# Performance work log

Measured on AMD Instinct MI355X. Metric: run time of the kernel, lower is better.

## Reference

```python
import jax, jax.numpy as jnp
import numpy as np

E, H, W = 1024, 16, 256  # embed_dim, num_heads, window_size
D = E // H               # head_dim


def _rmsnorm(t, w):
    eps = jnp.finfo(t.dtype).eps
    return t * jax.lax.rsqrt(jnp.mean(t * t, axis=-1, keepdims=True) + eps) * w


def setup_inputs() -> dict:
    key = jax.random.key(0)
    ks = jax.random.split(key, 11)
    B, T = 2, 2048
    s = 1.0 / np.sqrt(E)
    return {
        "x": jax.random.normal(ks[0], (B, T, E), jnp.float32),
        "wq": jax.random.normal(ks[1], (E, E), jnp.float32) * s,
        "bq": jnp.zeros((E,), jnp.float32),
        "wk": jax.random.normal(ks[2], (E, E), jnp.float32) * s,
        "bk": jnp.zeros((E,), jnp.float32),
        "wv": jax.random.normal(ks[3], (E, E), jnp.float32) * s,
        "bv": jnp.zeros((E,), jnp.float32),
        "wo": jax.random.normal(ks[4], (E, E), jnp.float32) * s,
        "bo": jnp.zeros((E,), jnp.float32),
        "qn_w": jnp.ones((D,), jnp.float32),
        "kn_w": jnp.ones((D,), jnp.float32),
    }


def reference(x, wq, bq, wk, bk, wv, bv, wo, bo, qn_w, kn_w):
    B, T, _ = x.shape
    # projections; weights stored (in, out)
    q = (x @ wq + bq).reshape(B, T, H, D).transpose(0, 2, 1, 3)  # [B,H,T,D]
    k = (x @ wk + bk).reshape(B, T, H, D).transpose(0, 2, 1, 3)
    v = (x @ wv + bv).reshape(B, T, H, D).transpose(0, 2, 1, 3)
    q = _rmsnorm(q, qn_w)
    k = _rmsnorm(k, kn_w)

    scores = jnp.einsum("bhqd,bhkd->bhqk", q, k) / jnp.sqrt(jnp.float32(D))
    row = jnp.arange(T)[:, None]
    col = jnp.arange(T)[None, :]
    invalid = (col > row) | (row - col >= W)  # causal + sliding window
    neg_inf = jnp.float32(-jnp.inf)
    scores = jnp.where(invalid, neg_inf, scores)

    # genetic fitness reweighting
    masked_attn = jnp.where(invalid, 0.0, jax.nn.softmax(scores, axis=-1))
    gene_means = jnp.mean(jax.nn.sigmoid(masked_attn), axis=-1)  # [B,H,T]
    denom = gene_means + 0.5
    sum_inv = jnp.sum(1.0 / denom, axis=2, keepdims=True)        # [B,H,1]
    fitness = 1.0 / (denom * sum_inv)                            # [B,H,T]
    scores = scores + jnp.log(fitness)[..., None]

    attn = jax.nn.softmax(scores, axis=-1)
    out = jnp.einsum("bhqk,bhkd->bhqd", attn, v)
    out = out.transpose(0, 2, 1, 3).reshape(B, T, E)
    return out @ wo + bo
```

## Files before the change

### kernel.cpp

```cpp
#include <hip/hip_runtime.h>

typedef _Float16 f16;
typedef _Float16 f16x4 __attribute__((ext_vector_type(4)));
typedef _Float16 f16x8 __attribute__((ext_vector_type(8)));
typedef float f32x4 __attribute__((ext_vector_type(4)));

#define MFMA16(a, b, c) __builtin_amdgcn_mfma_f32_16x16x32_f16(a, b, c, 0, 0, 0)

constexpr int T = 2048;
constexpr int E = 1024;
constexpr int H = 16;
constexpr int D = 64;
constexpr int WIN = 256;
#define NEGF (-1e30f)
#define L2E 1.4426950408889634f

__device__ __forceinline__ void gload16(const f16* g, f16* l) {
  __builtin_amdgcn_global_load_lds(
      (__attribute__((address_space(1))) void*)(void*)g,
      (__attribute__((address_space(3))) void*)(void*)l, 16, 0, 0);
}

__global__ __launch_bounds__(256) void cast_x_kernel(const float* __restrict__ x,
                                                     f16* __restrict__ xb) {
  int idx = (blockIdx.x * 256 + threadIdx.x) * 4;
  float4 v = *(const float4*)(x + idx);
  f16x4 o = {(f16)v.x, (f16)v.y, (f16)v.z, (f16)v.w};
  *(f16x4*)(xb + idx) = o;
}

__global__ __launch_bounds__(256) void transpose_w_kernel(
    const float* __restrict__ w0, const float* __restrict__ w1,
    const float* __restrict__ w2, const float* __restrict__ w3,
    f16* __restrict__ o0, f16* __restrict__ o1, f16* __restrict__ o2,
    f16* __restrict__ o3) {
  int z = blockIdx.z;
  const float* w = z == 0 ? w0 : z == 1 ? w1 : z == 2 ? w2 : w3;
  f16* o = z == 0 ? o0 : z == 1 ? o1 : z == 2 ? o2 : o3;
  __shared__ float tile[64][65];
  int k0 = blockIdx.x * 64, n0 = blockIdx.y * 64;
  int r = threadIdx.x >> 2, cb = (threadIdx.x & 3) * 16;
  const float* src = w + (size_t)(k0 + r) * E + n0 + cb;
#pragma unroll
  for (int j = 0; j < 16; j += 4) {
    float4 v = *(const float4*)(src + j);
    tile[r][cb + j] = v.x;
    tile[r][cb + j + 1] = v.y;
    tile[r][cb + j + 2] = v.z;
    tile[r][cb + j + 3] = v.w;
  }
  __syncthreads();
  f16 tmp[16];
#pragma unroll
  for (int j = 0; j < 16; ++j) tmp[j] = (f16)tile[cb + j][r];
  f16* dst = o + (size_t)(n0 + r) * E + k0 + cb;
  *(f16x8*)dst = *(f16x8*)&tmp[0];
  *(f16x8*)(dst + 8) = *(f16x8*)&tmp[8];
}

template <int QKV>
__global__ __launch_bounds__(256) void gemm_bt_kernel(
    const f16* __restrict__ A, const f16* __restrict__ B0,
    const f16* __restrict__ B1, const f16* __restrict__ B2,
    const float* __restrict__ c0, const float* __restrict__ c1,
    const float* __restrict__ c2, const float* __restrict__ qnw,
    const float* __restrict__ knw, f16* __restrict__ oq, f16* __restrict__ ok,
    f16* __restrict__ Vt, float* __restrict__ of32, int M, int N, int K) {
  int z = blockIdx.z;
  const f16* Bt = z == 0 ? B0 : z == 1 ? B1 : B2;
  const float* bias = z == 0 ? c0 : z == 1 ? c1 : c2;

  __shared__ f16 lA[2][8192];
  __shared__ f16 lB[2][8192];

  int sw = ((blockIdx.x & 7) << 5) + (blockIdx.x >> 3);
  int m0 = (sw >> 3) << 7, n0 = (sw & 7) << 7;

  int tid = threadIdx.x;
  int wid = tid >> 6, lane = tid & 63;
  int wm = wid >> 1, wn = wid & 1;
  int lr = lane & 15, lg = lane >> 4;

  f32x4 zero = {0.f, 0.f, 0.f, 0.f};
  f32x4 acc[4][4];
  for (int a = 0; a < 4; ++a)
    for (int b = 0; b < 4; ++b) acc[a][b] = zero;

  int srow = lane >> 3;
  int scol = (lane & 7) << 3;

  auto stage = [&](int buf, int k0) {
#pragma unroll
    for (int p = 0; p < 4; ++p) {
      int cc = (wid << 2) + p;
      int row = (cc << 3) + srow;
      int gc = scol ^ ((row & 7) << 3);
      gload16(A + (size_t)(m0 + row) * K + k0 + gc, &lA[buf][cc << 9]);
      gload16(Bt + (size_t)(n0 + row) * K + k0 + gc, &lB[buf][cc << 9]);
    }
  };

  int nit = K >> 6;
  stage(0, 0);
  __syncthreads();
  int cur = 0;
  for (int t = 0; t < nit; ++t) {
    if (t + 1 < nit) stage(cur ^ 1, (t + 1) << 6);
#pragma unroll
    for (int kk = 0; kk < 2; ++kk) {
      int kc = kk * 32 + (lg << 3);
      f16x8 af[4], bf[4];
#pragma unroll
      for (int mt = 0; mt < 4; ++mt) {
        int row = wm * 64 + mt * 16 + lr;
        af[mt] = *(const f16x8*)&lA[cur][((row << 6) + kc) ^ ((row & 7) << 3)];
      }
#pragma unroll
      for (int nt = 0; nt < 4; ++nt) {
        int row = wn * 64 + nt * 16 + lr;
        bf[nt] = *(const f16x8*)&lB[cur][((row << 6) + kc) ^ ((row & 7) << 3)];
      }
#pragma unroll
      for (int mt = 0; mt < 4; ++mt)
#pragma unroll
        for (int nt = 0; nt < 4; ++nt)
          acc[mt][nt] = MFMA16(af[mt], bf[nt], acc[mt][nt]);
    }
    if (t + 1 < nit) {
      __syncthreads();
      cur ^= 1;
    }
  }

  if constexpr (QKV == 1) {
    if (z < 2) {
      const float* nw = z == 0 ? qnw : knw;
      f16* o = z == 0 ? oq : ok;
      const float eps = 1.1920929e-7f;
      const float osc = z == 0 ? 0.125f : 1.0f;
      float wv_[4];
#pragma unroll
      for (int nt = 0; nt < 4; ++nt) wv_[nt] = nw[nt * 16 + lr] * osc;
#pragma unroll
      for (int mt = 0; mt < 4; ++mt) {
        float vbuf[4][4];
        float ss[4] = {0.f, 0.f, 0.f, 0.f};
#pragma unroll
        for (int nt = 0; nt < 4; ++nt) {
          float bv = bias[n0 + wn * 64 + nt * 16 + lr];
#pragma unroll
          for (int i = 0; i < 4; ++i) {
            float v = acc[mt][nt][i] + bv;
            vbuf[nt][i] = v;
            ss[i] += v * v;
          }
        }
        float rr[4];
#pragma unroll
        for (int i = 0; i < 4; ++i) {
          ss[i] += __shfl_xor(ss[i], 1);
          ss[i] += __shfl_xor(ss[i], 2);
          ss[i] += __shfl_xor(ss[i], 4);
          ss[i] += __shfl_xor(ss[i], 8);
          rr[i] = rsqrtf(ss[i] * (1.0f / 64.0f) + eps);
        }
        int row = m0 + wm * 64 + mt * 16 + (lg << 2);
#pragma unroll
        for (int nt = 0; nt < 4; ++nt) {
          int col = n0 + wn * 64 + nt * 16 + lr;
#pragma unroll
          for (int i = 0; i < 4; ++i)
            o[(size_t)(row + i) * N + col] = (f16)(vbuf[nt][i] * rr[i] * wv_[nt]);
        }
      }
    } else {
#pragma unroll
      for (int mt = 0; mt < 4; ++mt) {
        int row = m0 + wm * 64 + mt * 16 + (lg << 2);
        int b = row >> 11;
        int t = row & (T - 1);
#pragma unroll
        for (int nt = 0; nt < 4; ++nt) {
          int col = n0 + wn * 64 + nt * 16 + lr;
          float bv = bias[col];
          int h = col >> 6, d = col & 63;
          f16x4 pk = {(f16)(acc[mt][nt][0] + bv), (f16)(acc[mt][nt][1] + bv),
                      (f16)(acc[mt][nt][2] + bv), (f16)(acc[mt][nt][3] + bv)};
          *(f16x4*)&Vt[(((size_t)(b * H + h) * D + d) << 11) + t] = pk;
        }
      }
    }
  } else {
#pragma unroll
    for (int mt = 0; mt < 4; ++mt) {
#pragma unroll
      for (int nt = 0; nt < 4; ++nt) {
        int row = m0 + wm * 64 + mt * 16 + (lg << 2);
        int col = n0 + wn * 64 + nt * 16 + lr;
        float bv = bias[col];
#pragma unroll
        for (int i = 0; i < 4; ++i)
          of32[(size_t)(row + i) * N + col] = acc[mt][nt][i] + bv;
      }
    }
  }
}

__global__ __launch_bounds__(256) void attn_kernel(const f16* __restrict__ qn,
                                                   const f16* __restrict__ kn,
                                                   const f16* __restrict__ Vt,
                                                   f16* __restrict__ aout) {
  int sw = ((blockIdx.x & 7) << 7) + (blockIdx.x >> 3);
  int q0 = (sw & 31) << 6;
  int bh = sw >> 5;
  int b = bh >> 4, h = bh & 15;
  int tid = threadIdx.x;
  int w = tid >> 6, lane = tid & 63;
  int lr = lane & 15, lg = lane >> 4;

  __shared__ f16 lK[2][4096];
  __shared__ f16 lV[2][4096];
  __shared__ f16 lP[4096];

  const f16* Qb = qn + (size_t)(b * T + q0 + w * 16 + lr) * E + h * 64 + (lg << 3);
  f16x8 qf0 = *(const f16x8*)Qb;
  f16x8 qf1 = *(const f16x8*)(Qb + 32);

  f32x4 zero = {0.f, 0.f, 0.f, 0.f};
  f32x4 acc[4] = {zero, zero, zero, zero};
  float m[4] = {NEGF, NEGF, NEGF, NEGF};
  float l[4] = {0.f, 0.f, 0.f, 0.f};

  int mi = q0 >> 6;
  int kts = mi - 4 < 0 ? 0 : mi - 4;

  const f16* Kbase = kn + (size_t)b * T * E + h * 64;
  const f16* Vbase = Vt + (size_t)bh * D * T;

  int srow = lane >> 3;
  int scol = (lane & 7) << 3;

  auto stageKV = [&](int buf, int kt) {
    int k0 = kt << 6;
#pragma unroll
    for (int p = 0; p < 2; ++p) {
      int cc = (w << 1) + p;
      int row = (cc << 3) + srow;
      int gc = scol ^ ((row & 7) << 3);
      gload16(Kbase + (size_t)(k0 + row) * E + gc, &lK[buf][cc << 9]);
      gload16(Vbase + (size_t)row * T + k0 + gc, &lV[buf][cc << 9]);
    }
  };

  stageKV(0, kts);
  __syncthreads();
  int cur = 0;

  for (int kt = kts; kt <= mi; ++kt) {
    if (kt < mi) stageKV(cur ^ 1, kt + 1);
    int k0 = kt << 6;

    f32x4 s[4];
#pragma unroll
    for (int ct = 0; ct < 4; ++ct) s[ct] = zero;
#pragma unroll
    for (int kk = 0; kk < 2; ++kk) {
      int kc = kk * 32 + (lg << 3);
#pragma unroll
      for (int ct = 0; ct < 4; ++ct) {
        int row = ct * 16 + lr;
        f16x8 bf = *(const f16x8*)&lK[cur][((row << 6) + kc) ^ ((row & 7) << 3)];
        s[ct] = MFMA16(kk == 0 ? qf0 : qf1, bf, s[ct]);
      }
    }

    float tm[4] = {NEGF, NEGF, NEGF, NEGF};
    int rowg0 = q0 + w * 16 + (lg << 2);
    bool needmask = (kt == mi) || (mi >= 4 && kt == kts);
    if (needmask) {
#pragma unroll
      for (int ct = 0; ct < 4; ++ct) {
        int col = k0 + ct * 16 + lr;
#pragma unroll
        for (int i = 0; i < 4; ++i) {
          int rowg = rowg0 + i;
          float v = s[ct][i];
          if (col > rowg || rowg - col >= WIN) v = NEGF;
          s[ct][i] = v;
          tm[i] = fmaxf(tm[i], v);
        }
      }
    } else {
#pragma unroll
      for (int ct = 0; ct < 4; ++ct)
#pragma unroll
        for (int i = 0; i < 4; ++i) tm[i] = fmaxf(tm[i], s[ct][i]);
    }
#pragma unroll
    for (int i = 0; i < 4; ++i) {
      tm[i] = fmaxf(tm[i], __shfl_xor(tm[i], 1));
      tm[i] = fmaxf(tm[i], __shfl_xor(tm[i], 2));
      tm[i] = fmaxf(tm[i], __shfl_xor(tm[i], 4));
      tm[i] = fmaxf(tm[i], __shfl_xor(tm[i], 8));
    }
    bool up = (tm[0] > m[0]) || (tm[1] > m[1]) || (tm[2] > m[2]) ||
              (tm[3] > m[3]);
    if (__any(up)) {
      float fac[4];
#pragma unroll
      for (int i = 0; i < 4; ++i) {
        float mn = fmaxf(m[i], tm[i]);
        fac[i] = exp2f((m[i] - mn) * L2E);
        m[i] = mn;
        l[i] *= fac[i];
      }
#pragma unroll
      for (int dt = 0; dt < 4; ++dt)
#pragma unroll
        for (int i = 0; i < 4; ++i) acc[dt][i] *= fac[i];
    }
    float ps[4] = {0.f, 0.f, 0.f, 0.f};
#pragma unroll
    for (int ct = 0; ct < 4; ++ct)
#pragma unroll
      for (int i = 0; i < 4; ++i) {
        float p = exp2f((s[ct][i] - m[i]) * L2E);
        s[ct][i] = p;
        ps[i] += p;
      }
#pragma unroll
    for (int i = 0; i < 4; ++i) {
      ps[i] += __shfl_xor(ps[i], 1);
      ps[i] += __shfl_xor(ps[i], 2);
      ps[i] += __shfl_xor(ps[i], 4);
      ps[i] += __shfl_xor(ps[i], 8);
      l[i] += ps[i];
    }

#pragma unroll
    for (int ct = 0; ct < 4; ++ct)
#pragma unroll
      for (int i = 0; i < 4; ++i) {
        int qloc = (lg << 2) + i;
        int el = (qloc << 6) + ct * 16 + lr;
        lP[w * 1024 + (el ^ ((qloc & 7) << 3))] = (f16)s[ct][i];
      }

#pragma unroll
    for (int kk = 0; kk < 2; ++kk) {
      int kc = kk * 32 + (lg << 3);
      int ep = w * 1024 + (((lr << 6) + kc) ^ ((lr & 7) << 3));
      f16x8 pf = *(const f16x8*)&lP[ep];
#pragma unroll
      for (int dt = 0; dt < 4; ++dt) {
        int row = dt * 16 + lr;
        f16x8 vf = *(const f16x8*)&lV[cur][((row << 6) + kc) ^ ((row & 7) << 3)];
        acc[dt] = MFMA16(pf, vf, acc[dt]);
      }
    }

    if (kt < mi) {
      __syncthreads();
      cur ^= 1;
    }
  }

#pragma unroll
  for (int i = 0; i < 4; ++i) {
    float inv = 1.0f / l[i];
    int tok = q0 + w * 16 + (lg << 2) + i;
    f16* dst = aout + (size_t)(b * T + tok) * E + h * 64 + lr;
#pragma unroll
    for (int dt = 0; dt < 4; ++dt) dst[dt * 16] = (f16)(acc[dt][i] * inv);
  }
}

extern "C" void kernel_launch(void* const* d_in, const int* in_sizes, int n_in,
                              void* d_out, int out_size, void* d_ws,
                              size_t ws_size, hipStream_t stream) {
  const float* x = (const float*)d_in[0];
  const float* wq = (const float*)d_in[1];
  const float* bq = (const float*)d_in[2];
  const float* wk = (const float*)d_in[3];
  const float* bk = (const float*)d_in[4];
  const float* wv = (const float*)d_in[5];
  const float* bv = (const float*)d_in[6];
  const float* wo = (const float*)d_in[7];
  const float* bo = (const float*)d_in[8];
  const float* qn_w = (const float*)d_in[9];
  const float* kn_w = (const float*)d_in[10];
  float* out = (float*)d_out;

  char* ws = (char*)d_ws;
  const size_t MB = 1u << 20;
  f16* xb = (f16*)(ws);
  f16* wqT = (f16*)(ws + 8 * MB);
  f16* wkT = (f16*)(ws + 10 * MB);
  f16* wvT = (f16*)(ws + 12 * MB);
  f16* woT = (f16*)(ws + 14 * MB);
  f16* qn = (f16*)(ws + 16 * MB);
  f16* kn = (f16*)(ws + 24 * MB);
  f16* Vt = (f16*)(ws + 32 * MB);
  f16* aout = (f16*)(ws + 40 * MB);

  cast_x_kernel<<<4096, 256, 0, stream>>>(x, xb);
  transpose_w_kernel<<<dim3(16, 16, 4), 256, 0, stream>>>(wq, wk, wv, wo, wqT,
                                                          wkT, wvT, woT);
  gemm_bt_kernel<1><<<dim3(256, 1, 3), 256, 0, stream>>>(
      xb, wqT, wkT, wvT, bq, bk, bv, qn_w, kn_w, qn, kn, Vt, nullptr, 4096,
      1024, 1024);
  attn_kernel<<<1024, 256, 0, stream>>>(qn, kn, Vt, aout);
  gemm_bt_kernel<0><<<dim3(256, 1, 1), 256, 0, stream>>>(
      aout, woT, woT, woT, bo, bo, bo, nullptr, nullptr, nullptr, nullptr,
      nullptr, out, 4096, 1024, 1024);
}
```

Before: 105.7 us.

## Process 128 query rows per attention block to reuse staged K/V tiles

Each attention block now covers 128 queries instead of 64, with each wave handling two 16-row query subtiles. This halves the grid and lets every staged K/V tile in LDS serve twice as many queries, cutting global K/V traffic. Boundary tiles that only one half of the block needs are skipped per wave. In exchange, each block runs one extra K/V iteration and uses more registers and a larger P buffer, and the grid now has fewer blocks to spread across the GPU.

Result: no change. 107.6 us (+1.8%).

```diff
diff --git a/kernel.cpp b/kernel.cpp
--- a/kernel.cpp
+++ b/kernel.cpp
@@ -210,9 +210,9 @@
                                                    const f16* __restrict__ kn,
                                                    const f16* __restrict__ Vt,
                                                    f16* __restrict__ aout) {
-  int sw = ((blockIdx.x & 7) << 7) + (blockIdx.x >> 3);
-  int q0 = (sw & 31) << 6;
-  int bh = sw >> 5;
+  int sw = ((blockIdx.x & 7) << 6) + (blockIdx.x >> 3);
+  int q0 = (sw & 15) << 7;
+  int bh = sw >> 4;
   int b = bh >> 4, h = bh & 15;
   int tid = threadIdx.x;
   int w = tid >> 6, lane = tid & 63;
@@ -220,19 +220,31 @@
 
   __shared__ f16 lK[2][4096];
   __shared__ f16 lV[2][4096];
-  __shared__ f16 lP[4096];
-
-  const f16* Qb = qn + (size_t)(b * T + q0 + w * 16 + lr) * E + h * 64 + (lg << 3);
-  f16x8 qf0 = *(const f16x8*)Qb;
-  f16x8 qf1 = *(const f16x8*)(Qb + 32);
+  __shared__ f16 lP[8192];
+
+  const f16* Qb =
+      qn + (size_t)(b * T + q0 + w * 32 + lr) * E + h * 64 + (lg << 3);
+  f16x8 qf[2][2];
+  qf[0][0] = *(const f16x8*)Qb;
+  qf[0][1] = *(const f16x8*)(Qb + 32);
+  qf[1][0] = *(const f16x8*)(Qb + (size_t)16 * E);
+  qf[1][1] = *(const f16x8*)(Qb + (size_t)16 * E + 32);
 
   f32x4 zero = {0.f, 0.f, 0.f, 0.f};
-  f32x4 acc[4] = {zero, zero, zero, zero};
-  float m[4] = {NEGF, NEGF, NEGF, NEGF};
-  float l[4] = {0.f, 0.f, 0.f, 0.f};
-
-  int mi = q0 >> 6;
-  int kts = mi - 4 < 0 ? 0 : mi - 4;
+  f32x4 acc[2][4];
+  float m[2][4], l[2][4];
+#pragma unroll
+  for (int r = 0; r < 2; ++r)
+#pragma unroll
+    for (int i = 0; i < 4; ++i) {
+      acc[r][i] = zero;
+      m[r][i] = NEGF;
+      l[r][i] = 0.f;
+    }
+
+  int qt = q0 >> 6;
+  int kts = qt - 4 < 0 ? 0 : qt - 4;
+  int kte = qt + 1;
 
   const f16* Kbase = kn + (size_t)b * T * E + h * 64;
   const f16* Vbase = Vt + (size_t)bh * D * T;
@@ -256,123 +268,135 @@
   __syncthreads();
   int cur = 0;
 
-  for (int kt = kts; kt <= mi; ++kt) {
-    if (kt < mi) stageKV(cur ^ 1, kt + 1);
+  for (int kt = kts; kt <= kte; ++kt) {
+    if (kt < kte) stageKV(cur ^ 1, kt + 1);
     int k0 = kt << 6;
-
-    f32x4 s[4];
-#pragma unroll
-    for (int ct = 0; ct < 4; ++ct) s[ct] = zero;
-#pragma unroll
-    for (int kk = 0; kk < 2; ++kk) {
-      int kc = kk * 32 + (lg << 3);
-#pragma unroll
-      for (int ct = 0; ct < 4; ++ct) {
-        int row = ct * 16 + lr;
-        f16x8 bf = *(const f16x8*)&lK[cur][((row << 6) + kc) ^ ((row & 7) << 3)];
-        s[ct] = MFMA16(kk == 0 ? qf0 : qf1, bf, s[ct]);
-      }
-    }
-
-    float tm[4] = {NEGF, NEGF, NEGF, NEGF};
-    int rowg0 = q0 + w * 16 + (lg << 2);
-    bool needmask = (kt == mi) || (mi >= 4 && kt == kts);
-    if (needmask) {
-#pragma unroll
-      for (int ct = 0; ct < 4; ++ct) {
-        int col = k0 + ct * 16 + lr;
+    bool needmask = (kt <= qt - 3) || (kt >= qt);
+
+    bool skipwave = (kt == qt + 1 && w < 2) || (kt == qt - 4 && w >= 2);
+    if (!skipwave) {
+#pragma unroll
+      for (int r = 0; r < 2; ++r) {
+        f32x4 s[4];
+#pragma unroll
+        for (int ct = 0; ct < 4; ++ct) s[ct] = zero;
+#pragma unroll
+        for (int kk = 0; kk < 2; ++kk) {
+          int kc = kk * 32 + (lg << 3);
+#pragma unroll
+          for (int ct = 0; ct < 4; ++ct) {
+            int row = ct * 16 + lr;
+            f16x8 bf =
+                *(const f16x8*)&lK[cur][((row << 6) + kc) ^ ((row & 7) << 3)];
+            s[ct] = MFMA16(qf[r][kk], bf, s[ct]);
+          }
+        }
+
+        float tm[4] = {NEGF, NEGF, NEGF, NEGF};
+        int rowg0 = q0 + w * 32 + r * 16 + (lg << 2);
+        if (needmask) {
+#pragma unroll
+          for (int ct = 0; ct < 4; ++ct) {
+            int col = k0 + ct * 16 + lr;
+#pragma unroll
+            for (int i = 0; i < 4; ++i) {
+              int rowg = rowg0 + i;
+              float v = s[ct][i];
+              if (col > rowg || rowg - col >= WIN) v = NEGF;
+              s[ct][i] = v;
+              tm[i] = fmaxf(tm[i], v);
+            }
+          }
+        } else {
+#pragma unroll
+          for (int ct = 0; ct < 4; ++ct)
+#pragma unroll
+            for (int i = 0; i < 4; ++i) tm[i] = fmaxf(tm[i], s[ct][i]);
+        }
 #pragma unroll
         for (int i = 0; i < 4; ++i) {
-          int rowg = rowg0 + i;
-          float v = s[ct][i];
-          if (col > rowg || rowg - col >= WIN) v = NEGF;
-          s[ct][i] = v;
-          tm[i] = fmaxf(tm[i], v);
-        }
-      }
-    } else {
-#pragma unroll
-      for (int ct = 0; ct < 4; ++ct)
-#pragma unroll
-        for (int i = 0; i < 4; ++i) tm[i] = fmaxf(tm[i], s[ct][i]);
-    }
-#pragma unroll
-    for (int i = 0; i < 4; ++i) {
-      tm[i] = fmaxf(tm[i], __shfl_xor(tm[i], 1));
-      tm[i] = fmaxf(tm[i], __shfl_xor(tm[i], 2));
-      tm[i] = fmaxf(tm[i], __shfl_xor(tm[i], 4));
-      tm[i] = fmaxf(tm[i], __shfl_xor(tm[i], 8));
-    }
-    bool up = (tm[0] > m[0]) || (tm[1] > m[1]) || (tm[2] > m[2]) ||
-              (tm[3] > m[3]);
-    if (__any(up)) {
-      float fac[4];
-#pragma unroll
-      for (int i = 0; i < 4; ++i) {
-        float mn = fmaxf(m[i], tm[i]);
-        fac[i] = exp2f((m[i] - mn) * L2E);
-        m[i] = mn;
-        l[i] *= fac[i];
-      }
-#pragma unroll
-      for (int dt = 0; dt < 4; ++dt)
-#pragma unroll
-        for (int i = 0; i < 4; ++i) acc[dt][i] *= fac[i];
-    }
-    float ps[4] = {0.f, 0.f, 0.f, 0.f};
-#pragma unroll
-    for (int ct = 0; ct < 4; ++ct)
-#pragma unroll
-      for (int i = 0; i < 4; ++i) {
-        float p = exp2f((s[ct][i] - m[i]) * L2E);
-        s[ct][i] = p;
-        ps[i] += p;
-      }
-#pragma unroll
-    for (int i = 0; i < 4; ++i) {
-      ps[i] += __shfl_xor(ps[i], 1);
-      ps[i] += __shfl_xor(ps[i], 2);
-      ps[i] += __shfl_xor(ps[i], 4);
-      ps[i] += __shfl_xor(ps[i], 8);
-      l[i] += ps[i];
-    }
-
-#pragma unroll
-    for (int ct = 0; ct < 4; ++ct)
-#pragma unroll
-      for (int i = 0; i < 4; ++i) {
-        int qloc = (lg << 2) + i;
-        int el = (qloc << 6) + ct * 16 + lr;
-        lP[w * 1024 + (el ^ ((qloc & 7) << 3))] = (f16)s[ct][i];
-      }
-
-#pragma unroll
-    for (int kk = 0; kk < 2; ++kk) {
-      int kc = kk * 32 + (lg << 3);
-      int ep = w * 1024 + (((lr << 6) + kc) ^ ((lr & 7) << 3));
-      f16x8 pf = *(const f16x8*)&lP[ep];
-#pragma unroll
-      for (int dt = 0; dt < 4; ++dt) {
-        int row = dt * 16 + lr;
-        f16x8 vf = *(const f16x8*)&lV[cur][((row << 6) + kc) ^ ((row & 7) << 3)];
-        acc[dt] = MFMA16(pf, vf, acc[dt]);
-      }
-    }
-
-    if (kt < mi) {
+          tm[i] = fmaxf(tm[i], __shfl_xor(tm[i], 1));
+          tm[i] = fmaxf(tm[i], __shfl_xor(tm[i], 2));
+          tm[i] = fmaxf(tm[i], __shfl_xor(tm[i], 4));
+          tm[i] = fmaxf(tm[i], __shfl_xor(tm[i], 8));
+        }
+        bool up = (tm[0] > m[r][0]) || (tm[1] > m[r][1]) ||
+                  (tm[2] > m[r][2]) || (tm[3] > m[r][3]);
+        if (__any(up)) {
+          float fac[4];
+#pragma unroll
+          for (int i = 0; i < 4; ++i) {
+            float mn = fmaxf(m[r][i], tm[i]);
+            fac[i] = exp2f((m[r][i] - mn) * L2E);
+            m[r][i] = mn;
+            l[r][i] *= fac[i];
+          }
+#pragma unroll
+          for (int dt = 0; dt < 4; ++dt)
+#pragma unroll
+            for (int i = 0; i < 4; ++i) acc[r][dt][i] *= fac[i];
+        }
+        float ps[4] = {0.f, 0.f, 0.f, 0.f};
+#pragma unroll
+        for (int ct = 0; ct < 4; ++ct)
+#pragma unroll
+          for (int i = 0; i < 4; ++i) {
+            float p = exp2f((s[ct][i] - m[r][i]) * L2E);
+            s[ct][i] = p;
+            ps[i] += p;
+          }
+#pragma unroll
+        for (int i = 0; i < 4; ++i) {
+          ps[i] += __shfl_xor(ps[i], 1);
+          ps[i] += __shfl_xor(ps[i], 2);
+          ps[i] += __shfl_xor(ps[i], 4);
+          ps[i] += __shfl_xor(ps[i], 8);
+          l[r][i] += ps[i];
+        }
+
+        int pbase = w * 2048 + r * 1024;
+#pragma unroll
+        for (int ct = 0; ct < 4; ++ct)
+#pragma unroll
+          for (int i = 0; i < 4; ++i) {
+            int qloc = (lg << 2) + i;
+            int el = (qloc << 6) + ct * 16 + lr;
+            lP[pbase + (el ^ ((qloc & 7) << 3))] = (f16)s[ct][i];
+          }
+
+#pragma unroll
+        for (int kk = 0; kk < 2; ++kk) {
+          int kc = kk * 32 + (lg << 3);
+          int ep = pbase + (((lr << 6) + kc) ^ ((lr & 7) << 3));
+          f16x8 pf = *(const f16x8*)&lP[ep];
+#pragma unroll
+          for (int dt = 0; dt < 4; ++dt) {
+            int row = dt * 16 + lr;
+            f16x8 vf =
+                *(const f16x8*)&lV[cur][((row << 6) + kc) ^ ((row & 7) << 3)];
+            acc[r][dt] = MFMA16(pf, vf, acc[r][dt]);
+          }
+        }
+      }
+    }
+
+    if (kt < kte) {
       __syncthreads();
       cur ^= 1;
     }
   }
 
 #pragma unroll
-  for (int i = 0; i < 4; ++i) {
-    float inv = 1.0f / l[i];
-    int tok = q0 + w * 16 + (lg << 2) + i;
-    f16* dst = aout + (size_t)(b * T + tok) * E + h * 64 + lr;
-#pragma unroll
-    for (int dt = 0; dt < 4; ++dt) dst[dt * 16] = (f16)(acc[dt][i] * inv);
-  }
+  for (int r = 0; r < 2; ++r)
+#pragma unroll
+    for (int i = 0; i < 4; ++i) {
+      float inv = 1.0f / l[r][i];
+      int tok = q0 + w * 32 + r * 16 + (lg << 2) + i;
+      f16* dst = aout + (size_t)(b * T + tok) * E + h * 64 + lr;
+#pragma unroll
+      for (int dt = 0; dt < 4; ++dt)
+        dst[dt * 16] = (f16)(acc[r][dt][i] * inv);
+    }
 }
 
 extern "C" void kernel_launch(void* const* d_in, const int* in_sizes, int n_in,
@@ -409,7 +433,7 @@
   gemm_bt_kernel<1><<<dim3(256, 1, 3), 256, 0, stream>>>(
       xb, wqT, wkT, wvT, bq, bk, bv, qn_w, kn_w, qn, kn, Vt, nullptr, 4096,
       1024, 1024);
-  attn_kernel<<<1024, 256, 0, stream>>>(qn, kn, Vt, aout);
+  attn_kernel<<<512, 256, 0, stream>>>(qn, kn, Vt, aout);
   gemm_bt_kernel<0><<<dim3(256, 1, 1), 256, 0, stream>>>(
       aout, woT, woT, woT, bo, bo, bo, nullptr, nullptr, nullptr, nullptr,
       nullptr, out, 4096, 1024, 1024);
```
